# Kernel optimization log

Hardware: AMD Instinct MI355X
Metric: run time of the kernel (lower is better)

## Reference

```python
import jax, jax.numpy as jnp
import numpy as np

N_NODES = 10000
N_EDGES = 160000
IN_CH = 1030
HID = 256
HEADS = 4
OUT_CH = 49
NEG_SLOPE = 0.2
EPS = 1e-5


def setup_inputs() -> dict:
    key = jax.random.key(0)
    ks = jax.random.split(key, 20)
    HC = HID * HEADS  # 1024
    inp = {
        "x": jax.random.normal(ks[0], (N_NODES, IN_CH), dtype=jnp.float32),
        "edge_index": jax.random.randint(ks[1], (2, N_EDGES), 0, N_NODES, dtype=jnp.int64),
        # conv1 (GATv2): lin_l (source), lin_r (target), att, out bias
        "c1_wl": jax.random.normal(ks[2], (IN_CH, HC), dtype=jnp.float32) * 0.03,
        "c1_bl": jnp.zeros((HC,), dtype=jnp.float32),
        "c1_wr": jax.random.normal(ks[3], (IN_CH, HC), dtype=jnp.float32) * 0.03,
        "c1_br": jnp.zeros((HC,), dtype=jnp.float32),
        "c1_att": jax.random.normal(ks[4], (HEADS, HID), dtype=jnp.float32) * 0.06,
        "c1_bias": jnp.zeros((HC,), dtype=jnp.float32),
        # norm1 (per-node LayerNorm over channels)
        "ln1_w": jnp.ones((HC,), dtype=jnp.float32),
        "ln1_b": jnp.zeros((HC,), dtype=jnp.float32),
        # conv2
        "c2_wl": jax.random.normal(ks[5], (HC, HC), dtype=jnp.float32) * 0.03,
        "c2_bl": jnp.zeros((HC,), dtype=jnp.float32),
        "c2_wr": jax.random.normal(ks[6], (HC, HC), dtype=jnp.float32) * 0.03,
        "c2_br": jnp.zeros((HC,), dtype=jnp.float32),
        "c2_att": jax.random.normal(ks[7], (HEADS, HID), dtype=jnp.float32) * 0.06,
        "c2_bias": jnp.zeros((HC,), dtype=jnp.float32),
        # norm2
        "ln2_w": jnp.ones((HC,), dtype=jnp.float32),
        "ln2_b": jnp.zeros((HC,), dtype=jnp.float32),
        # classifier: Linear(HC, HID) -> ELU -> Linear(HID, OUT_CH)
        "cls_w1": jax.random.normal(ks[8], (HC, HID), dtype=jnp.float32) * 0.03,
        "cls_b1": jnp.zeros((HID,), dtype=jnp.float32),
        "cls_w2": jax.random.normal(ks[9], (HID, OUT_CH), dtype=jnp.float32) * 0.06,
        "cls_b2": jnp.zeros((OUT_CH,), dtype=jnp.float32),
    }
    return inp


def gatv2_conv(x, src, dst, wl, bl, wr, br, att, bias, n_nodes):
    """PyG GATv2Conv, concat heads. src/dst include self loops."""
    H, C = att.shape
    xl = (x @ wl + bl).reshape(-1, H, C)  # source transform [N,H,C]
    xr = (x @ wr + br).reshape(-1, H, C)  # target transform [N,H,C]
    m = xl[src] + xr[dst]                  # [E,H,C] gather + add
    e = jnp.einsum("ehc,hc->eh", jax.nn.leaky_relu(m, NEG_SLOPE), att)  # [E,H]
    # segment softmax over destination node
    emax = jax.ops.segment_max(e, dst, num_segments=n_nodes)
    p = jnp.exp(e - emax[dst])
    denom = jax.ops.segment_sum(p, dst, num_segments=n_nodes)
    alpha = p / (denom[dst] + 1e-16)       # [E,H]
    out = jax.ops.segment_sum(xl[src] * alpha[:, :, None], dst, num_segments=n_nodes)
    return out.reshape(n_nodes, H * C) + bias


def layer_norm(x, w, b):
    mu = jnp.mean(x, axis=-1, keepdims=True)
    var = jnp.var(x, axis=-1, keepdims=True)
    return (x - mu) / jnp.sqrt(var + EPS) * w + b


def reference(x, edge_index, c1_wl, c1_bl, c1_wr, c1_br, c1_att, c1_bias,
              ln1_w, ln1_b, c2_wl, c2_bl, c2_wr, c2_br, c2_att, c2_bias,
              ln2_w, ln2_b, cls_w1, cls_b1, cls_w2, cls_b2):
    n = x.shape[0]
    loops = jnp.arange(n, dtype=edge_index.dtype)
    src = jnp.concatenate([edge_index[0], loops])  # add_self_loops=True
    dst = jnp.concatenate([edge_index[1], loops])

    h = gatv2_conv(x, src, dst, c1_wl, c1_bl, c1_wr, c1_br, c1_att, c1_bias, n)
    h = jax.nn.elu(layer_norm(h, ln1_w, ln1_b))
    # dropout: identity at inference
    h = gatv2_conv(h, src, dst, c2_wl, c2_bl, c2_wr, c2_br, c2_att, c2_bias, n)
    h = jax.nn.elu(layer_norm(h, ln2_w, ln2_b))
    h = jax.nn.elu(h @ cls_w1 + cls_b1)
    return h @ cls_w2 + cls_b2  # [N, 49]
```

## Files before the change

### kernel.cpp

```cpp
#include <hip/hip_runtime.h>
#include <stdint.h>

#define N_NODES 10000
#define N_EDGES 160000
#define E_TOT   170000
#define IN_CH   1030
#define HC      1024
#define OUT_CH  49
#define NEG_SLOPE 0.2f
#define LN_EPS 1e-5f
#define LOG2E 1.4426950408889634f

#define MPAD  10112
#define K1PAD 1088

typedef __attribute__((ext_vector_type(8))) __bf16 bf16x8;
typedef __attribute__((ext_vector_type(4))) float floatx4;
typedef __attribute__((ext_vector_type(2))) float floatx2;
typedef _Float16 h2 __attribute__((ext_vector_type(2)));

static __device__ __forceinline__ unsigned short f2bf(float f) {
  union { float f; uint32_t u; } v; v.f = f;
  uint32_t u = v.u;
  u += 0x7fffu + ((u >> 16) & 1u);
  return (unsigned short)(u >> 16);
}
static __device__ __forceinline__ unsigned short f2h(float f) {
  _Float16 h = (_Float16)f;
  union { _Float16 h; unsigned short u; } v; v.h = h; return v.u;
}
static __device__ __forceinline__ h2 bits2h2(uint32_t u) {
  union { uint32_t i; h2 h; } v; v.i = u; return v.h;
}
static __device__ __forceinline__ floatx2 h2f2(h2 a) {
  floatx2 r; r.x = (float)a.x; r.y = (float)a.y; return r;
}

static __device__ __forceinline__ float wred_add(float x) {
#define DPP_ADD(ctrl, rmask)                                                   \
  x += __builtin_bit_cast(float, __builtin_amdgcn_update_dpp(                  \
           0, __builtin_bit_cast(int, x), ctrl, rmask, 0xf, true))
  DPP_ADD(0x111, 0xf);
  DPP_ADD(0x112, 0xf);
  DPP_ADD(0x114, 0xf);
  DPP_ADD(0x118, 0xf);
  DPP_ADD(0x142, 0xa);
  DPP_ADD(0x143, 0xc);
#undef DPP_ADD
  return __builtin_bit_cast(float,
      __builtin_amdgcn_readlane(__builtin_bit_cast(int, x), 63));
}


__global__ void cast_x_kernel(const float* __restrict__ x, unsigned short* __restrict__ xa,
                              int* __restrict__ counts) {
  int idx = blockIdx.x * 256 + threadIdx.x;
  if (idx < N_NODES) counts[idx] = 0;
  if (idx >= N_NODES * K1PAD) return;
  int m = idx / K1PAD, k = idx - m * K1PAD;
  float v = (k < IN_CH) ? x[m * IN_CH + k] : 0.f;
  xa[idx] = f2bf(v);
}

static __device__ __forceinline__ void transpose_body(
    float (*tile)[33], const float* __restrict__ wa, const float* __restrict__ wb,
    int split, int lda, int ldb, int Kvalid, int Kout,
    unsigned short* __restrict__ out, int bx, int by, int t) {
  int n0 = bx * 32, k0 = by * 32;
  int tx = t & 31, ty = t >> 5;
#pragma unroll
  for (int i = 0; i < 4; i++) {
    int k = k0 + ty + i * 8;
    int n = n0 + tx;
    float v = 0.f;
    if (k < Kvalid) v = (n < split) ? wa[(size_t)k * lda + n] : wb[(size_t)k * ldb + (n - split)];
    tile[ty + i * 8][tx] = v;
  }
  __syncthreads();
#pragma unroll
  for (int i = 0; i < 4; i++) {
    int n = n0 + ty + i * 8;
    int k = k0 + tx;
    out[(size_t)n * Kout + k] = f2bf(tile[tx][ty + i * 8]);
  }
}

#define NB_W1 2176
#define NB_W2 2048
#define NB_WC 256
#define NB_CNT 665
__global__ __launch_bounds__(256) void prep2_kernel(
    const float* __restrict__ c1_wl, const float* __restrict__ c1_wr,
    const float* __restrict__ c2_wl, const float* __restrict__ c2_wr,
    const float* __restrict__ cls_w1,
    const int* __restrict__ dstArr, int* __restrict__ counts,
    unsigned short* __restrict__ wt1, unsigned short* __restrict__ wt2,
    unsigned short* __restrict__ wtc1)
{
  __shared__ float tile[32][33];
  int b = blockIdx.x, t = threadIdx.x;
  if (b < NB_W1) {
    transpose_body(tile, c1_wl, c1_wr, 1024, 1024, 1024, IN_CH, K1PAD, wt1, b & 63, b >> 6, t);
  } else if (b < NB_W1 + NB_W2) {
    int bb = b - NB_W1;
    transpose_body(tile, c2_wl, c2_wr, 1024, 1024, 1024, 1024, 1024, wt2, bb & 63, bb >> 6, t);
  } else if (b < NB_W1 + NB_W2 + NB_WC) {
    int bb = b - (NB_W1 + NB_W2);
    transpose_body(tile, cls_w1, cls_w1, 256, 256, 256, 1024, 1024, wtc1, bb & 7, bb >> 3, t);
  } else {
    int e = (b - (NB_W1 + NB_W2 + NB_WC)) * 256 + t;
    if (e < E_TOT) {
      int d = (e < N_EDGES) ? dstArr[e] : (e - N_EDGES);
      atomicAdd(&counts[d], 1);
    }
  }
}

__global__ __launch_bounds__(256) void scan_kernel(const int* __restrict__ counts,
                                                   int* __restrict__ rstart,
                                                   int* __restrict__ rwork) {
  __shared__ int sm[256];
  int t = threadIdx.x;
  int b0 = t * 40;
  int b1 = b0 + 40; if (b1 > N_NODES) b1 = N_NODES; if (b0 > N_NODES) b0 = N_NODES;
  int s = 0;
  for (int i = b0; i < b1; i++) s += counts[i];
  sm[t] = s; __syncthreads();
  for (int st = 1; st < 256; st <<= 1) {
    int add = (t >= st) ? sm[t - st] : 0;
    __syncthreads();
    sm[t] += add;
    __syncthreads();
  }
  int run = sm[t] - s;
  for (int i = b0; i < b1; i++) { rstart[i] = run; rwork[i] = run; run += counts[i]; }
  if (t == 255) rstart[N_NODES] = run;
}

__global__ void scatter_kernel(const int* __restrict__ srcArr, const int* __restrict__ dstArr,
                               int* __restrict__ rwork, int* __restrict__ csrsrc) {
  int e = blockIdx.x * 256 + threadIdx.x;
  if (e >= E_TOT) return;
  if (e < 16) csrsrc[E_TOT + e] = 0;
  int d, sv;
  if (e < N_EDGES) { d = dstArr[e]; sv = srcArr[e]; }
  else { d = e - N_EDGES; sv = d; }
  int pos = atomicAdd(&rwork[d], 1);
  csrsrc[pos] = sv;
}

template <int MODE, int KC>
__global__ __launch_bounds__(256, 4) void gemm_bf16(
    const unsigned short* __restrict__ A, const unsigned short* __restrict__ Bt,
    float* __restrict__ Cf, unsigned short* __restrict__ Cb,
    const float* __restrict__ blo, const float* __restrict__ bhi,
    int M, int ldc, int bsplit)
{
  __shared__ __align__(16) unsigned short As[128 * 64];
  __shared__ __align__(16) unsigned short Bs[128 * 64];
  const int t = threadIdx.x;
  const int w = t >> 6, lane = t & 63;

  const unsigned int nwg = gridDim.x * gridDim.y;
  const unsigned int bid = blockIdx.y * gridDim.x + blockIdx.x;
  const unsigned int q8 = nwg >> 3, r8 = nwg & 7;
  const unsigned int xcd = bid & 7, sub = bid >> 3;
  const unsigned int wg = (xcd < r8 ? xcd * (q8 + 1) : r8 * (q8 + 1) + (xcd - r8) * q8) + sub;
  const int tile_n = (wg % gridDim.x) * 128, tile_m = (wg / gridDim.x) * 128;

  floatx4 acc[4][4] = {};

  const int qq = w * 64 + lane;
  const int row0 = qq >> 3;
  const int gj = (qq & 7) ^ (row0 & 7);
  const unsigned short* gA0 = A  + (size_t)(tile_m + row0) * KC + gj * 8;
  const unsigned short* gB0 = Bt + (size_t)(tile_n + row0) * KC + gj * 8;

  const int wm = (w >> 1) * 64, wn = (w & 1) * 64;
  const int lrow = lane & 15, cg0 = (lane >> 4);
  const int sw = lrow & 7;

#pragma unroll 1
  for (int k0 = 0; k0 < KC; k0 += 64) {
#pragma unroll
    for (int p = 0; p < 4; p++) {
      __builtin_amdgcn_global_load_lds(
          (const __attribute__((address_space(1))) void*)(gA0 + p * 32 * KC),
          (__attribute__((address_space(3))) void*)(As + p * 2048 + w * 512), 16, 0, 0);
      __builtin_amdgcn_global_load_lds(
          (const __attribute__((address_space(1))) void*)(gB0 + p * 32 * KC),
          (__attribute__((address_space(3))) void*)(Bs + p * 2048 + w * 512), 16, 0, 0);
    }
    gA0 += 64; gB0 += 64;
    __syncthreads();
#pragma unroll
    for (int h = 0; h < 2; h++) {
      const int sc = (h * 4 + cg0) ^ sw;
      bf16x8 a[4], b[4];
#pragma unroll
      for (int mi = 0; mi < 4; mi++)
        a[mi] = *(const bf16x8*)(As + (wm + mi * 16 + lrow) * 64 + sc * 8);
#pragma unroll
      for (int ni = 0; ni < 4; ni++)
        b[ni] = *(const bf16x8*)(Bs + (wn + ni * 16 + lrow) * 64 + sc * 8);
#pragma unroll
      for (int mi = 0; mi < 4; mi++)
#pragma unroll
        for (int ni = 0; ni < 4; ni++)
          acc[mi][ni] = __builtin_amdgcn_mfma_f32_16x16x32_bf16(a[mi], b[ni], acc[mi][ni], 0, 0, 0);
    }
    __syncthreads();
  }

  float bcol[4];
#pragma unroll
  for (int ni = 0; ni < 4; ni++) {
    int n = tile_n + wn + ni * 16 + lrow;
    bcol[ni] = (n < bsplit) ? blo[n] : bhi[n - bsplit];
  }

  const int rbase = (lane >> 4) * 4;
#pragma unroll
  for (int mi = 0; mi < 4; mi++) {
#pragma unroll
    for (int r = 0; r < 4; r++) {
      int m = tile_m + wm + mi * 16 + rbase + r;
      if (m >= M) continue;
#pragma unroll
      for (int ni = 0; ni < 4; ni++) {
        int n = tile_n + wn + ni * 16 + lrow;
        float v = acc[mi][ni][r] + bcol[ni];
        if (MODE == 0) {
          Cf[(size_t)m * ldc + n] = v;
        } else if (MODE == 1) {
          Cf[(size_t)m * ldc + n] = v > 0.f ? v : expm1f(v);
        } else {
          Cb[(size_t)m * 2048 + n] = f2h(v);
        }
      }
    }
  }
}


__global__ __launch_bounds__(256) void gat_ln_kernel(
    const unsigned short* __restrict__ xlr,
    const float* __restrict__ att,
    const int* __restrict__ csrsrc, const int* __restrict__ rstart,
    const float* __restrict__ bias,
    const float* __restrict__ lnw, const float* __restrict__ lnb,
    unsigned short* __restrict__ out)
{
  const int d = blockIdx.x;
  const int t = threadIdx.x;
  const int lane = t & 63, wv = t >> 6;
  const int c = wv * 256 + lane * 4;

  uint2 xru = *(const uint2*)(xlr + (size_t)d * 2048 + 1024 + c);
  h2 xr0 = bits2h2(xru.x), xr1 = bits2h2(xru.y);
  float4 aw4 = *(const float4*)(att + c);
  h2 aw0, aw1;
  aw0.x = (_Float16)(aw4.x * LOG2E); aw0.y = (_Float16)(aw4.y * LOG2E);
  aw1.x = (_Float16)(aw4.z * LOG2E); aw1.y = (_Float16)(aw4.w * LOG2E);
  const h2 ns = {(_Float16)NEG_SLOPE, (_Float16)NEG_SLOPE};
  const unsigned short* xbase = xlr + c;

  int start = rstart[d], deg = rstart[d + 1] - start;

  float m = -3.0e38f, l = 0.f;
  floatx2 accA = {0.f, 0.f}, accB = {0.f, 0.f};

  int i = 0;
  if (deg >= 4) {
    int sA0 = csrsrc[start],     sA1 = csrsrc[start + 1];
    int sA2 = csrsrc[start + 2], sA3 = csrsrc[start + 3];
    uint2 uA0 = *(const uint2*)(xbase + (size_t)sA0 * 2048);
    uint2 uA1 = *(const uint2*)(xbase + (size_t)sA1 * 2048);
    uint2 uA2 = *(const uint2*)(xbase + (size_t)sA2 * 2048);
    uint2 uA3 = *(const uint2*)(xbase + (size_t)sA3 * 2048);
    int sB0 = csrsrc[start + 4], sB1 = csrsrc[start + 5];
    int sB2 = csrsrc[start + 6], sB3 = csrsrc[start + 7];
    for (; i + 4 <= deg; i += 4) {
      int sC0 = csrsrc[start + i + 8],  sC1 = csrsrc[start + i + 9];
      int sC2 = csrsrc[start + i + 10], sC3 = csrsrc[start + i + 11];
      uint2 uB0 = *(const uint2*)(xbase + (size_t)sB0 * 2048);
      uint2 uB1 = *(const uint2*)(xbase + (size_t)sB1 * 2048);
      uint2 uB2 = *(const uint2*)(xbase + (size_t)sB2 * 2048);
      uint2 uB3 = *(const uint2*)(xbase + (size_t)sB3 * 2048);

      h2 xh0a = bits2h2(uA0.x), xh0b = bits2h2(uA0.y);
      h2 xh1a = bits2h2(uA1.x), xh1b = bits2h2(uA1.y);
      h2 xh2a = bits2h2(uA2.x), xh2b = bits2h2(uA2.y);
      h2 xh3a = bits2h2(uA3.x), xh3b = bits2h2(uA3.y);
      h2 t0a = xh0a + xr0, t0b = xh0b + xr1;
      h2 t1a = xh1a + xr0, t1b = xh1b + xr1;
      h2 t2a = xh2a + xr0, t2b = xh2b + xr1;
      h2 t3a = xh3a + xr0, t3b = xh3b + xr1;
      h2 r0a = __builtin_elementwise_max(t0a, t0a * ns);
      h2 r0b = __builtin_elementwise_max(t0b, t0b * ns);
      h2 r1a = __builtin_elementwise_max(t1a, t1a * ns);
      h2 r1b = __builtin_elementwise_max(t1b, t1b * ns);
      h2 r2a = __builtin_elementwise_max(t2a, t2a * ns);
      h2 r2b = __builtin_elementwise_max(t2b, t2b * ns);
      h2 r3a = __builtin_elementwise_max(t3a, t3a * ns);
      h2 r3b = __builtin_elementwise_max(t3b, t3b * ns);
      float p0 = __builtin_amdgcn_fdot2(r0b, aw1, __builtin_amdgcn_fdot2(r0a, aw0, 0.f, false), false);
      float p1 = __builtin_amdgcn_fdot2(r1b, aw1, __builtin_amdgcn_fdot2(r1a, aw0, 0.f, false), false);
      float p2 = __builtin_amdgcn_fdot2(r2b, aw1, __builtin_amdgcn_fdot2(r2a, aw0, 0.f, false), false);
      float p3 = __builtin_amdgcn_fdot2(r3b, aw1, __builtin_amdgcn_fdot2(r3a, aw0, 0.f, false), false);
      p0 = wred_add(p0);
      p1 = wred_add(p1);
      p2 = wred_add(p2);
      p3 = wred_add(p3);
      float mx = fmaxf(fmaxf(p0, p1), fmaxf(p2, p3));
      if (mx > m) {
        float sc = exp2f(m - mx);
        floatx2 scv; scv.x = sc; scv.y = sc;
        accA *= scv; accB *= scv; l *= sc;
        m = mx;
      }
      float pe0 = exp2f(p0 - m), pe1 = exp2f(p1 - m);
      float pe2 = exp2f(p2 - m), pe3 = exp2f(p3 - m);
      floatx2 x0A = h2f2(xh0a), x0B = h2f2(xh0b);
      floatx2 x1A = h2f2(xh1a), x1B = h2f2(xh1b);
      floatx2 x2A = h2f2(xh2a), x2B = h2f2(xh2b);
      floatx2 x3A = h2f2(xh3a), x3B = h2f2(xh3b);
      floatx2 v0; v0.x = pe0; v0.y = pe0;
      floatx2 v1; v1.x = pe1; v1.y = pe1;
      floatx2 v2; v2.x = pe2; v2.y = pe2;
      floatx2 v3; v3.x = pe3; v3.y = pe3;
      accA += x0A * v0; accA += x1A * v1; accA += x2A * v2; accA += x3A * v3;
      accB += x0B * v0; accB += x1B * v1; accB += x2B * v2; accB += x3B * v3;
      l += pe0 + pe1 + pe2 + pe3;

      uA0 = uB0; uA1 = uB1; uA2 = uB2; uA3 = uB3;
      sB0 = sC0; sB1 = sC1; sB2 = sC2; sB3 = sC3;
    }
  }
  for (; i < deg; i++) {
    int s0 = csrsrc[start + i];
    uint2 u0 = *(const uint2*)(xbase + (size_t)s0 * 2048);
    h2 xh0a = bits2h2(u0.x), xh0b = bits2h2(u0.y);
    h2 t0a = xh0a + xr0, t0b = xh0b + xr1;
    h2 r0a = __builtin_elementwise_max(t0a, t0a * ns);
    h2 r0b = __builtin_elementwise_max(t0b, t0b * ns);
    float p0 = __builtin_amdgcn_fdot2(r0b, aw1, __builtin_amdgcn_fdot2(r0a, aw0, 0.f, false), false);
    p0 = wred_add(p0);
    if (p0 > m) {
      float sc = exp2f(m - p0);
      floatx2 scv; scv.x = sc; scv.y = sc;
      accA *= scv; accB *= scv; l *= sc;
      m = p0;
    }
    float pe0 = exp2f(p0 - m);
    floatx2 x0A = h2f2(xh0a), x0B = h2f2(xh0b);
    floatx2 pe0v; pe0v.x = pe0; pe0v.y = pe0;
    accA += x0A * pe0v;
    accB += x0B * pe0v;
    l += pe0;
  }

  float rd = 1.f / (l + 1e-16f);
  float4 bv = *(const float4*)(bias + c);
  float o0 = accA.x * rd + bv.x, o1 = accA.y * rd + bv.y;
  float o2 = accB.x * rd + bv.z, o3 = accB.y * rd + bv.w;

  __shared__ float ws1[4], ws2[4];
  float s1 = o0 + o1 + o2 + o3;
  float s2 = o0 * o0 + o1 * o1 + o2 * o2 + o3 * o3;
#pragma unroll
  for (int mm = 32; mm >= 1; mm >>= 1) {
    s1 += __shfl_xor(s1, mm, 64);
    s2 += __shfl_xor(s2, mm, 64);
  }
  if (lane == 0) { ws1[wv] = s1; ws2[wv] = s2; }
  __syncthreads();
  float mean = (ws1[0] + ws1[1] + ws1[2] + ws1[3]) * (1.f / 1024.f);
  float var  = (ws2[0] + ws2[1] + ws2[2] + ws2[3]) * (1.f / 1024.f) - mean * mean;
  float rstd = rsqrtf(var + LN_EPS);
  float4 wv4 = *(const float4*)(lnw + c);
  float4 bb  = *(const float4*)(lnb + c);
  float z0 = (o0 - mean) * rstd * wv4.x + bb.x; z0 = z0 > 0.f ? z0 : expm1f(z0);
  float z1 = (o1 - mean) * rstd * wv4.y + bb.y; z1 = z1 > 0.f ? z1 : expm1f(z1);
  float z2 = (o2 - mean) * rstd * wv4.z + bb.z; z2 = z2 > 0.f ? z2 : expm1f(z2);
  float z3 = (o3 - mean) * rstd * wv4.w + bb.w; z3 = z3 > 0.f ? z3 : expm1f(z3);
  ushort4 u;
  u.x = f2bf(z0); u.y = f2bf(z1); u.z = f2bf(z2); u.w = f2bf(z3);
  *(ushort4*)(out + (size_t)d * 1024 + c) = u;
}


__global__ __launch_bounds__(256) void cls2_kernel(
    const float* __restrict__ h3, const float* __restrict__ w2,
    const float* __restrict__ b2, float* __restrict__ out)
{
  __shared__ float row[4][256];
  int t = threadIdx.x, wv = t >> 6, lane = t & 63;
  int node = blockIdx.x * 4 + wv;
  *(float4*)(&row[wv][lane * 4]) = *(const float4*)(h3 + (size_t)node * 256 + lane * 4);
  __syncthreads();
  if (lane < OUT_CH) {
    float a0 = 0.f, a1 = 0.f, a2 = 0.f, a3 = 0.f;
#pragma unroll 4
    for (int k = 0; k < 256; k += 4) {
      a0 += row[wv][k]     * w2[(k    ) * OUT_CH + lane];
      a1 += row[wv][k + 1] * w2[(k + 1) * OUT_CH + lane];
      a2 += row[wv][k + 2] * w2[(k + 2) * OUT_CH + lane];
      a3 += row[wv][k + 3] * w2[(k + 3) * OUT_CH + lane];
    }
    out[node * OUT_CH + lane] = (a0 + a1) + (a2 + a3) + b2[lane];
  }
}


extern "C" void kernel_launch(void* const* d_in, const int* in_sizes, int n_in,
                              void* d_out, int out_size, void* d_ws, size_t ws_size,
                              hipStream_t stream)
{
  const float* x       = (const float*)d_in[0];
  const int*   ei      = (const int*)d_in[1];
  const float* c1_wl   = (const float*)d_in[2];
  const float* c1_bl   = (const float*)d_in[3];
  const float* c1_wr   = (const float*)d_in[4];
  const float* c1_br   = (const float*)d_in[5];
  const float* c1_att  = (const float*)d_in[6];
  const float* c1_bias = (const float*)d_in[7];
  const float* ln1_w   = (const float*)d_in[8];
  const float* ln1_b   = (const float*)d_in[9];
  const float* c2_wl   = (const float*)d_in[10];
  const float* c2_bl   = (const float*)d_in[11];
  const float* c2_wr   = (const float*)d_in[12];
  const float* c2_br   = (const float*)d_in[13];
  const float* c2_att  = (const float*)d_in[14];
  const float* c2_bias = (const float*)d_in[15];
  const float* ln2_w   = (const float*)d_in[16];
  const float* ln2_b   = (const float*)d_in[17];
  const float* cls_w1  = (const float*)d_in[18];
  const float* cls_b1  = (const float*)d_in[19];
  const float* cls_w2  = (const float*)d_in[20];
  const float* cls_b2  = (const float*)d_in[21];

  const int* srcArr = ei;
  const int* dstArr = ei + N_EDGES;

  char* ws = (char*)d_ws;
  size_t off = 0;
  auto alloc = [&](size_t bytes) { void* p = ws + off; off += (bytes + 255) & ~(size_t)255; return p; };
  unsigned short* xa      = (unsigned short*)alloc((size_t)MPAD * K1PAD * 2);
  unsigned short* wt1     = (unsigned short*)alloc((size_t)2048 * K1PAD * 2);
  unsigned short* wt2     = (unsigned short*)alloc((size_t)2048 * 1024 * 2);
  unsigned short* wtc1    = (unsigned short*)alloc((size_t)256 * 1024 * 2);
  unsigned short* xlr     = (unsigned short*)alloc((size_t)N_NODES * 2048 * 2);
  float*          h3      = (float*)alloc((size_t)N_NODES * 256 * 4);
  unsigned short* hb      = (unsigned short*)alloc((size_t)MPAD * 1024 * 2);
  int*            counts  = (int*)alloc(N_NODES * 4);
  int*            rwork   = (int*)alloc(N_NODES * 4);
  int*            rstart  = (int*)alloc((N_NODES + 1) * 4);
  int*            csrsrc  = (int*)alloc((E_TOT + 16) * 4);
  (void)in_sizes; (void)n_in; (void)out_size; (void)ws_size;

  cast_x_kernel<<<(N_NODES * K1PAD + 255) / 256, 256, 0, stream>>>(x, xa, counts);
  prep2_kernel<<<NB_W1 + NB_W2 + NB_WC + NB_CNT, 256, 0, stream>>>(
      c1_wl, c1_wr, c2_wl, c2_wr, cls_w1, dstArr, counts, wt1, wt2, wtc1);

  scan_kernel<<<1, 256, 0, stream>>>(counts, rstart, rwork);
  scatter_kernel<<<(E_TOT + 255) / 256, 256, 0, stream>>>(srcArr, dstArr, rwork, csrsrc);

  gemm_bf16<2, K1PAD><<<dim3(16, 79), 256, 0, stream>>>(xa, wt1, nullptr, xlr, c1_bl, c1_br, N_NODES, 0, 1024);
  gat_ln_kernel<<<N_NODES, 256, 0, stream>>>(xlr, c1_att, csrsrc, rstart, c1_bias, ln1_w, ln1_b, hb);

  gemm_bf16<2, 1024><<<dim3(16, 79), 256, 0, stream>>>(hb, wt2, nullptr, xlr, c2_bl, c2_br, N_NODES, 0, 1024);
  gat_ln_kernel<<<N_NODES, 256, 0, stream>>>(xlr, c2_att, csrsrc, rstart, c2_bias, ln2_w, ln2_b, hb);

  gemm_bf16<1, 1024><<<dim3(2, 79), 256, 0, stream>>>(hb, wtc1, h3, nullptr, cls_b1, cls_b1, N_NODES, 256, 1024);
  cls2_kernel<<<2500, 256, 0, stream>>>(h3, cls_w2, cls_b2, (float*)d_out);
}
```

Before: 458.6 us.

## Add 128x256-tile 512-thread GEMM with LDS double buffering for GAT projections

Adds a new bf16 MFMA GEMM kernel that uses 128x256 output tiles, 8 waves, direct global-to-LDS loads, a double-buffered K pipeline with explicit waitcnt and barrier scheduling, and XCD-aware tile mapping. It replaces the 128x128 GEMM for both GAT layer projections. The larger N tile raises operand reuse and halves A-tile reloads, and the pipelining overlaps loads with MFMA work. The output buffer is padded to MPAD rows because the new kernel writes without bounds checks. The 96KB of dynamic LDS and 512 threads per block may limit occupancy.

```diff
diff --git a/kernel.cpp b/kernel.cpp
--- a/kernel.cpp
+++ b/kernel.cpp
@@ -147,6 +147,137 @@
   else { d = e - N_EDGES; sv = d; }
   int pos = atomicAdd(&rwork[d], 1);
   csrsrc[pos] = sv;
+}
+
+
+extern __shared__ unsigned short smem256[];
+
+template <int KC>
+__global__ __launch_bounds__(512, 2) void gemm256(
+    const unsigned short* __restrict__ A,
+    const unsigned short* __restrict__ Bt,
+    unsigned short* __restrict__ Cb,
+    const float* __restrict__ blo, const float* __restrict__ bhi)
+{
+  constexpr int NT = KC / 64;
+  unsigned short* As = smem256;
+  unsigned short* Bs = smem256 + 2 * 8192;
+
+  const int tid = threadIdx.x;
+  const int w = tid >> 6, lane = tid & 63;
+  const int wm = w >> 2, wn = w & 3;
+
+  const unsigned int bid = blockIdx.y * gridDim.x + blockIdx.x;
+  const unsigned int wg = (bid & 7) * 79u + (bid >> 3);
+  const int tile_n = (int)(wg % 8u) * 256;
+  const int tile_m = (int)(wg / 8u) * 128;
+
+  const int rq = tid >> 3;
+  const int gc = (tid & 7) ^ (rq & 7);
+  const unsigned short* gA = A  + (size_t)(tile_m + rq) * KC + gc * 8;
+  const unsigned short* gB = Bt + (size_t)(tile_n + rq) * KC + gc * 8;
+  const int ldsw = w * 512;
+
+  const int lrow = lane & 15, cg0 = lane >> 4, sw = lrow & 7;
+
+  floatx4 acc[4][4] = {};
+
+#define STAGE_A(kt, p2)                                                          \
+  __builtin_amdgcn_global_load_lds(                                              \
+      (const __attribute__((address_space(1))) void*)(gA + (size_t)(p2) * 64 * KC + (kt) * 64), \
+      (__attribute__((address_space(3))) void*)(As + ((kt) & 1) * 8192 + (p2) * 4096 + ldsw), 16, 0, 0)
+#define STAGE_B(kt, s)                                                           \
+  __builtin_amdgcn_global_load_lds(                                              \
+      (const __attribute__((address_space(1))) void*)(gB + (size_t)(s) * 64 * KC + (kt) * 64),  \
+      (__attribute__((address_space(3))) void*)(Bs + ((kt) & 1) * 16384 + (s) * 4096 + ldsw), 16, 0, 0)
+
+  STAGE_B(0, 0); STAGE_B(0, 1); STAGE_A(0, 0);
+  STAGE_B(0, 2); STAGE_B(0, 3); STAGE_A(0, 1);
+
+  bf16x8 b[4][2], a[2][2];
+
+#pragma unroll 1
+  for (int t = 0; t < NT; ++t) {
+    const unsigned short* Ac = As + (t & 1) * 8192;
+    const unsigned short* Bc = Bs + (t & 1) * 16384;
+    const bool st = (t + 1 < NT);
+
+    asm volatile("s_waitcnt vmcnt(1)" ::: "memory");
+    __builtin_amdgcn_s_barrier();
+    asm volatile("" ::: "memory");
+    __builtin_amdgcn_sched_barrier(0);
+
+#pragma unroll
+    for (int n = 0; n < 4; ++n)
+#pragma unroll
+      for (int kh = 0; kh < 2; ++kh)
+        b[n][kh] = *(const bf16x8*)(Bc + (wn * 64 + n * 16 + lrow) * 64 + (((kh << 2) | cg0) ^ sw) * 8);
+#pragma unroll
+    for (int f = 0; f < 2; ++f)
+#pragma unroll
+      for (int kh = 0; kh < 2; ++kh)
+        a[f][kh] = *(const bf16x8*)(Ac + (f * 32 + wm * 16 + lrow) * 64 + (((kh << 2) | cg0) ^ sw) * 8);
+    if (st) { STAGE_B(t + 1, 0); STAGE_B(t + 1, 1); STAGE_A(t + 1, 0); }
+    __builtin_amdgcn_s_barrier();
+    asm volatile("s_waitcnt lgkmcnt(0)" ::: "memory");
+    __builtin_amdgcn_sched_barrier(0);
+    __builtin_amdgcn_s_setprio(1);
+#pragma unroll
+    for (int f = 0; f < 2; ++f)
+#pragma unroll
+      for (int n = 0; n < 4; ++n) {
+        acc[f][n] = __builtin_amdgcn_mfma_f32_16x16x32_bf16(a[f][0], b[n][0], acc[f][n], 0, 0, 0);
+        acc[f][n] = __builtin_amdgcn_mfma_f32_16x16x32_bf16(a[f][1], b[n][1], acc[f][n], 0, 0, 0);
+      }
+    __builtin_amdgcn_s_setprio(0);
+
+    if (st) asm volatile("s_waitcnt vmcnt(3)" ::: "memory");
+    else    asm volatile("s_waitcnt vmcnt(0)" ::: "memory");
+    __builtin_amdgcn_s_barrier();
+    asm volatile("" ::: "memory");
+    __builtin_amdgcn_sched_barrier(0);
+
+#pragma unroll
+    for (int f = 0; f < 2; ++f)
+#pragma unroll
+      for (int kh = 0; kh < 2; ++kh)
+        a[f][kh] = *(const bf16x8*)(Ac + ((f + 2) * 32 + wm * 16 + lrow) * 64 + (((kh << 2) | cg0) ^ sw) * 8);
+    if (st) { STAGE_B(t + 1, 2); STAGE_B(t + 1, 3); STAGE_A(t + 1, 1); }
+    __builtin_amdgcn_s_barrier();
+    asm volatile("s_waitcnt lgkmcnt(0)" ::: "memory");
+    __builtin_amdgcn_sched_barrier(0);
+    __builtin_amdgcn_s_setprio(1);
+#pragma unroll
+    for (int f = 0; f < 2; ++f)
+#pragma unroll
+      for (int n = 0; n < 4; ++n) {
+        acc[f + 2][n] = __builtin_amdgcn_mfma_f32_16x16x32_bf16(a[f][0], b[n][0], acc[f + 2][n], 0, 0, 0);
+        acc[f + 2][n] = __builtin_amdgcn_mfma_f32_16x16x32_bf16(a[f][1], b[n][1], acc[f + 2][n], 0, 0, 0);
+      }
+    __builtin_amdgcn_s_setprio(0);
+  }
+#undef STAGE_A
+#undef STAGE_B
+
+  const int rbase = cg0 * 4;
+  float bcol[4];
+#pragma unroll
+  for (int n = 0; n < 4; ++n) {
+    int col = tile_n + wn * 64 + n * 16 + lrow;
+    bcol[n] = (col < 1024) ? blo[col] : bhi[col - 1024];
+  }
+#pragma unroll
+  for (int f = 0; f < 4; ++f) {
+    const int mrow = tile_m + f * 32 + wm * 16 + rbase;
+#pragma unroll
+    for (int r = 0; r < 4; ++r) {
+#pragma unroll
+      for (int n = 0; n < 4; ++n) {
+        int col = tile_n + wn * 64 + n * 16 + lrow;
+        Cb[(size_t)(mrow + r) * 2048 + col] = f2h(acc[f][n][r] + bcol[n]);
+      }
+    }
+  }
 }
 
 template <int MODE, int KC>
@@ -450,7 +581,7 @@
   unsigned short* wt1     = (unsigned short*)alloc((size_t)2048 * K1PAD * 2);
   unsigned short* wt2     = (unsigned short*)alloc((size_t)2048 * 1024 * 2);
   unsigned short* wtc1    = (unsigned short*)alloc((size_t)256 * 1024 * 2);
-  unsigned short* xlr     = (unsigned short*)alloc((size_t)N_NODES * 2048 * 2);
+  unsigned short* xlr     = (unsigned short*)alloc((size_t)MPAD * 2048 * 2);
   float*          h3      = (float*)alloc((size_t)N_NODES * 256 * 4);
   unsigned short* hb      = (unsigned short*)alloc((size_t)MPAD * 1024 * 2);
   int*            counts  = (int*)alloc(N_NODES * 4);
@@ -466,10 +597,10 @@
   scan_kernel<<<1, 256, 0, stream>>>(counts, rstart, rwork);
   scatter_kernel<<<(E_TOT + 255) / 256, 256, 0, stream>>>(srcArr, dstArr, rwork, csrsrc);
 
-  gemm_bf16<2, K1PAD><<<dim3(16, 79), 256, 0, stream>>>(xa, wt1, nullptr, xlr, c1_bl, c1_br, N_NODES, 0, 1024);
+  gemm256<K1PAD><<<dim3(8, 79), 512, 98304, stream>>>(xa, wt1, xlr, c1_bl, c1_br);
   gat_ln_kernel<<<N_NODES, 256, 0, stream>>>(xlr, c1_att, csrsrc, rstart, c1_bias, ln1_w, ln1_b, hb);
 
-  gemm_bf16<2, 1024><<<dim3(16, 79), 256, 0, stream>>>(hb, wt2, nullptr, xlr, c2_bl, c2_br, N_NODES, 0, 1024);
+  gemm256<1024><<<dim3(8, 79), 512, 98304, stream>>>(hb, wt2, xlr, c2_bl, c2_br);
   gat_ln_kernel<<<N_NODES, 256, 0, stream>>>(xlr, c2_att, csrsrc, rstart, c2_bias, ln2_w, ln2_b, hb);
 
   gemm_bf16<1, 1024><<<dim3(2, 79), 256, 0, stream>>>(hb, wtc1, h3, nullptr, cls_b1, cls_b1, N_NODES, 256, 1024);
```

Result: slower. 490.9 us (+7.0%).

## Fuse classifier MLP into one MFMA kernel and vectorize input cast

Applied to the files above, without the earlier changes.

Replaces the classifier's bf16 GEMM plus scalar second-layer kernel with one kernel. It computes the first linear layer with MFMA, applies bias and ELU, stages the fp16 result in LDS, and does the second 256x49 layer with f16 MFMA against a pre-transposed padded weight. This removes the fp32 intermediate round trip through global memory and one launch, at the cost of fewer, larger blocks (79 blocks of 128 rows). The x-to-bf16 cast kernel is also vectorized to process four elements per thread.

```diff
diff --git a/kernel.cpp b/kernel.cpp
--- a/kernel.cpp
+++ b/kernel.cpp
@@ -15,6 +15,7 @@
 #define K1PAD 1088
 
 typedef __attribute__((ext_vector_type(8))) __bf16 bf16x8;
+typedef __attribute__((ext_vector_type(8))) _Float16 h8;
 typedef __attribute__((ext_vector_type(4))) float floatx4;
 typedef __attribute__((ext_vector_type(2))) float floatx2;
 typedef _Float16 h2 __attribute__((ext_vector_type(2)));
@@ -56,16 +57,27 @@
                               int* __restrict__ counts) {
   int idx = blockIdx.x * 256 + threadIdx.x;
   if (idx < N_NODES) counts[idx] = 0;
-  if (idx >= N_NODES * K1PAD) return;
-  int m = idx / K1PAD, k = idx - m * K1PAD;
-  float v = (k < IN_CH) ? x[m * IN_CH + k] : 0.f;
-  xa[idx] = f2bf(v);
+  if (idx >= N_NODES * (K1PAD / 4)) return;
+  int m = idx / (K1PAD / 4), k4 = idx - m * (K1PAD / 4);
+  int k = k4 * 4;
+  ushort4 o;
+  if (k + 3 < IN_CH) {
+    float2 v0 = *(const float2*)(x + (size_t)m * IN_CH + k);
+    float2 v1 = *(const float2*)(x + (size_t)m * IN_CH + k + 2);
+    o.x = f2bf(v0.x); o.y = f2bf(v0.y); o.z = f2bf(v1.x); o.w = f2bf(v1.y);
+  } else {
+    o.x = (k     < IN_CH) ? f2bf(x[(size_t)m * IN_CH + k    ]) : (unsigned short)0;
+    o.y = (k + 1 < IN_CH) ? f2bf(x[(size_t)m * IN_CH + k + 1]) : (unsigned short)0;
+    o.z = (k + 2 < IN_CH) ? f2bf(x[(size_t)m * IN_CH + k + 2]) : (unsigned short)0;
+    o.w = (unsigned short)0;
+  }
+  *(ushort4*)(xa + (size_t)m * K1PAD + k) = o;
 }
 
 static __device__ __forceinline__ void transpose_body(
     float (*tile)[33], const float* __restrict__ wa, const float* __restrict__ wb,
     int split, int lda, int ldb, int Kvalid, int Kout,
-    unsigned short* __restrict__ out, int bx, int by, int t) {
+    unsigned short* __restrict__ out, int bx, int by, int t, bool f16o) {
   int n0 = bx * 32, k0 = by * 32;
   int tx = t & 31, ty = t >> 5;
 #pragma unroll
@@ -73,7 +85,10 @@
     int k = k0 + ty + i * 8;
     int n = n0 + tx;
     float v = 0.f;
-    if (k < Kvalid) v = (n < split) ? wa[(size_t)k * lda + n] : wb[(size_t)k * ldb + (n - split)];
+    if (k < Kvalid) {
+      if (n < split) v = wa[(size_t)k * lda + n];
+      else if (ldb)  v = wb[(size_t)k * ldb + (n - split)];
+    }
     tile[ty + i * 8][tx] = v;
   }
   __syncthreads();
@@ -81,34 +96,39 @@
   for (int i = 0; i < 4; i++) {
     int n = n0 + ty + i * 8;
     int k = k0 + tx;
-    out[(size_t)n * Kout + k] = f2bf(tile[tx][ty + i * 8]);
+    float v = tile[tx][ty + i * 8];
+    out[(size_t)n * Kout + k] = f16o ? f2h(v) : f2bf(v);
   }
 }
 
 #define NB_W1 2176
 #define NB_W2 2048
 #define NB_WC 256
+#define NB_WC2 16
 #define NB_CNT 665
 __global__ __launch_bounds__(256) void prep2_kernel(
     const float* __restrict__ c1_wl, const float* __restrict__ c1_wr,
     const float* __restrict__ c2_wl, const float* __restrict__ c2_wr,
-    const float* __restrict__ cls_w1,
+    const float* __restrict__ cls_w1, const float* __restrict__ cls_w2,
     const int* __restrict__ dstArr, int* __restrict__ counts,
     unsigned short* __restrict__ wt1, unsigned short* __restrict__ wt2,
-    unsigned short* __restrict__ wtc1)
+    unsigned short* __restrict__ wtc1, unsigned short* __restrict__ wtc2)
 {
   __shared__ float tile[32][33];
   int b = blockIdx.x, t = threadIdx.x;
   if (b < NB_W1) {
-    transpose_body(tile, c1_wl, c1_wr, 1024, 1024, 1024, IN_CH, K1PAD, wt1, b & 63, b >> 6, t);
+    transpose_body(tile, c1_wl, c1_wr, 1024, 1024, 1024, IN_CH, K1PAD, wt1, b & 63, b >> 6, t, false);
   } else if (b < NB_W1 + NB_W2) {
     int bb = b - NB_W1;
-    transpose_body(tile, c2_wl, c2_wr, 1024, 1024, 1024, 1024, 1024, wt2, bb & 63, bb >> 6, t);
+    transpose_body(tile, c2_wl, c2_wr, 1024, 1024, 1024, 1024, 1024, wt2, bb & 63, bb >> 6, t, false);
   } else if (b < NB_W1 + NB_W2 + NB_WC) {
     int bb = b - (NB_W1 + NB_W2);
-    transpose_body(tile, cls_w1, cls_w1, 256, 256, 256, 1024, 1024, wtc1, bb & 7, bb >> 3, t);
+    transpose_body(tile, cls_w1, cls_w1, 256, 256, 256, 1024, 1024, wtc1, bb & 7, bb >> 3, t, false);
+  } else if (b < NB_W1 + NB_W2 + NB_WC + NB_WC2) {
+    int bb = b - (NB_W1 + NB_W2 + NB_WC);
+    transpose_body(tile, cls_w2, cls_w2, OUT_CH, OUT_CH, 0, 256, 256, wtc2, bb & 1, bb >> 1, t, true);
   } else {
-    int e = (b - (NB_W1 + NB_W2 + NB_WC)) * 256 + t;
+    int e = (b - (NB_W1 + NB_W2 + NB_WC + NB_WC2)) * 256 + t;
     if (e < E_TOT) {
       int d = (e < N_EDGES) ? dstArr[e] : (e - N_EDGES);
       atomicAdd(&counts[d], 1);
@@ -390,25 +410,127 @@
 }
 
 
-__global__ __launch_bounds__(256) void cls2_kernel(
-    const float* __restrict__ h3, const float* __restrict__ w2,
-    const float* __restrict__ b2, float* __restrict__ out)
+extern __shared__ unsigned short clssm[];
+
+__global__ __launch_bounds__(256) void cls_fused_kernel(
+    const unsigned short* __restrict__ A,
+    const unsigned short* __restrict__ Bt,
+    const float* __restrict__ b1,
+    const unsigned short* __restrict__ w2t,
+    const float* __restrict__ b2,
+    float* __restrict__ out)
 {
-  __shared__ float row[4][256];
-  int t = threadIdx.x, wv = t >> 6, lane = t & 63;
-  int node = blockIdx.x * 4 + wv;
-  *(float4*)(&row[wv][lane * 4]) = *(const float4*)(h3 + (size_t)node * 256 + lane * 4);
+  unsigned short* As = clssm;
+  unsigned short* Bs = clssm + 8192;
+  unsigned short* hbuf = clssm;
+
+  const int t = threadIdx.x;
+  const int w = t >> 6, lane = t & 63;
+  const int tile_m = blockIdx.x * 128;
+
+  const int q = w * 64 + lane;
+  const int row0 = q >> 3;
+  const int gj = (q & 7) ^ (row0 & 7);
+  const unsigned short* gA0 = A  + (size_t)(tile_m + row0) * 1024 + gj * 8;
+  const unsigned short* gB0 = Bt + (size_t)row0 * 1024 + gj * 8;
+
+  const int wm = (w >> 1) * 64, wn = (w & 1) * 128;
+  const int lrow = lane & 15, cg0 = lane >> 4, sw = lrow & 7;
+
+  floatx4 acc[4][8] = {};
+
+#pragma unroll 1
+  for (int k0 = 0; k0 < 1024; k0 += 64) {
+#pragma unroll
+    for (int p = 0; p < 4; p++)
+      __builtin_amdgcn_global_load_lds(
+          (const __attribute__((address_space(1))) void*)(gA0 + p * 32 * 1024),
+          (__attribute__((address_space(3))) void*)(As + p * 2048 + w * 512), 16, 0, 0);
+#pragma unroll
+    for (int s = 0; s < 8; s++)
+      __builtin_amdgcn_global_load_lds(
+          (const __attribute__((address_space(1))) void*)(gB0 + s * 32 * 1024),
+          (__attribute__((address_space(3))) void*)(Bs + s * 2048 + w * 512), 16, 0, 0);
+    gA0 += 64; gB0 += 64;
+    __syncthreads();
+#pragma unroll
+    for (int h = 0; h < 2; h++) {
+      const int sc = ((h << 2) | cg0) ^ sw;
+      bf16x8 a[4], b[8];
+#pragma unroll
+      for (int mi = 0; mi < 4; mi++) {
+        int ar = wm + mi * 16 + lrow;
+        a[mi] = *(const bf16x8*)(As + (ar >> 5) * 2048 + (ar & 31) * 64 + sc * 8);
+      }
+#pragma unroll
+      for (int ni = 0; ni < 8; ni++) {
+        int br = wn + ni * 16 + lrow;
+        b[ni] = *(const bf16x8*)(Bs + (br >> 5) * 2048 + (br & 31) * 64 + sc * 8);
+      }
+#pragma unroll
+      for (int mi = 0; mi < 4; mi++)
+#pragma unroll
+        for (int ni = 0; ni < 8; ni++)
+          acc[mi][ni] = __builtin_amdgcn_mfma_f32_16x16x32_bf16(a[mi], b[ni], acc[mi][ni], 0, 0, 0);
+    }
+    __syncthreads();
+  }
+
+  float bcol[8];
+#pragma unroll
+  for (int ni = 0; ni < 8; ni++) bcol[ni] = b1[wn + ni * 16 + lrow];
+  const int rbase = cg0 * 4;
+#pragma unroll
+  for (int mi = 0; mi < 4; mi++) {
+#pragma unroll
+    for (int r = 0; r < 4; r++) {
+      int row = wm + mi * 16 + rbase + r;
+#pragma unroll
+      for (int ni = 0; ni < 8; ni++) {
+        int col = wn + ni * 16 + lrow;
+        float v = acc[mi][ni][r] + bcol[ni];
+        v = v > 0.f ? v : expm1f(v);
+        int kc = (col >> 3) ^ (row & 7);
+        hbuf[row * 256 + kc * 8 + (col & 7)] = f2h(v);
+      }
+    }
+  }
   __syncthreads();
-  if (lane < OUT_CH) {
-    float a0 = 0.f, a1 = 0.f, a2 = 0.f, a3 = 0.f;
-#pragma unroll 4
-    for (int k = 0; k < 256; k += 4) {
-      a0 += row[wv][k]     * w2[(k    ) * OUT_CH + lane];
-      a1 += row[wv][k + 1] * w2[(k + 1) * OUT_CH + lane];
-      a2 += row[wv][k + 2] * w2[(k + 2) * OUT_CH + lane];
-      a3 += row[wv][k + 3] * w2[(k + 3) * OUT_CH + lane];
-    }
-    out[node * OUT_CH + lane] = (a0 + a1) + (a2 + a3) + b2[lane];
+
+  floatx4 acc3[2][4] = {};
+#pragma unroll
+  for (int kst = 0; kst < 8; kst++) {
+    h8 a3[2], b3[4];
+#pragma unroll
+    for (int mi = 0; mi < 2; mi++) {
+      int ar = w * 32 + mi * 16 + lrow;
+      int kc = (kst * 4 + cg0) ^ (ar & 7);
+      a3[mi] = *(const h8*)(hbuf + ar * 256 + kc * 8);
+    }
+#pragma unroll
+    for (int ni = 0; ni < 4; ni++) {
+      int br = ni * 16 + lrow;
+      b3[ni] = *(const h8*)(w2t + br * 256 + kst * 32 + cg0 * 8);
+    }
+#pragma unroll
+    for (int mi = 0; mi < 2; mi++)
+#pragma unroll
+      for (int ni = 0; ni < 4; ni++)
+        acc3[mi][ni] = __builtin_amdgcn_mfma_f32_16x16x32_f16(a3[mi], b3[ni], acc3[mi][ni], 0, 0, 0);
+  }
+#pragma unroll
+  for (int mi = 0; mi < 2; mi++) {
+    int rb = tile_m + w * 32 + mi * 16 + rbase;
+#pragma unroll
+    for (int r = 0; r < 4; r++) {
+      int node = rb + r;
+      if (node >= N_NODES) continue;
+#pragma unroll
+      for (int ni = 0; ni < 4; ni++) {
+        int j = ni * 16 + lrow;
+        if (j < OUT_CH) out[(size_t)node * OUT_CH + j] = acc3[mi][ni][r] + b2[j];
+      }
+    }
   }
 }
 
@@ -450,8 +572,8 @@
   unsigned short* wt1     = (unsigned short*)alloc((size_t)2048 * K1PAD * 2);
   unsigned short* wt2     = (unsigned short*)alloc((size_t)2048 * 1024 * 2);
   unsigned short* wtc1    = (unsigned short*)alloc((size_t)256 * 1024 * 2);
+  unsigned short* wtc2    = (unsigned short*)alloc((size_t)64 * 256 * 2);
   unsigned short* xlr     = (unsigned short*)alloc((size_t)N_NODES * 2048 * 2);
-  float*          h3      = (float*)alloc((size_t)N_NODES * 256 * 4);
   unsigned short* hb      = (unsigned short*)alloc((size_t)MPAD * 1024 * 2);
   int*            counts  = (int*)alloc(N_NODES * 4);
   int*            rwork   = (int*)alloc(N_NODES * 4);
@@ -459,9 +581,9 @@
   int*            csrsrc  = (int*)alloc((E_TOT + 16) * 4);
   (void)in_sizes; (void)n_in; (void)out_size; (void)ws_size;
 
-  cast_x_kernel<<<(N_NODES * K1PAD + 255) / 256, 256, 0, stream>>>(x, xa, counts);
-  prep2_kernel<<<NB_W1 + NB_W2 + NB_WC + NB_CNT, 256, 0, stream>>>(
-      c1_wl, c1_wr, c2_wl, c2_wr, cls_w1, dstArr, counts, wt1, wt2, wtc1);
+  cast_x_kernel<<<(N_NODES * (K1PAD / 4) + 255) / 256, 256, 0, stream>>>(x, xa, counts);
+  prep2_kernel<<<NB_W1 + NB_W2 + NB_WC + NB_WC2 + NB_CNT, 256, 0, stream>>>(
+      c1_wl, c1_wr, c2_wl, c2_wr, cls_w1, cls_w2, dstArr, counts, wt1, wt2, wtc1, wtc2);
 
   scan_kernel<<<1, 256, 0, stream>>>(counts, rstart, rwork);
   scatter_kernel<<<(E_TOT + 255) / 256, 256, 0, stream>>>(srcArr, dstArr, rwork, csrsrc);
@@ -472,6 +594,5 @@
   gemm_bf16<2, 1024><<<dim3(16, 79), 256, 0, stream>>>(hb, wt2, nullptr, xlr, c2_bl, c2_br, N_NODES, 0, 1024);
   gat_ln_kernel<<<N_NODES, 256, 0, stream>>>(xlr, c2_att, csrsrc, rstart, c2_bias, ln2_w, ln2_b, hb);
 
-  gemm_bf16<1, 1024><<<dim3(2, 79), 256, 0, stream>>>(hb, wtc1, h3, nullptr, cls_b1, cls_b1, N_NODES, 256, 1024);
-  cls2_kernel<<<2500, 256, 0, stream>>>(h3, cls_w2, cls_b2, (float*)d_out);
-}
+  cls_fused_kernel<<<79, 256, 65536, stream>>>(hb, wtc1, cls_b1, wtc2, cls_b2, (float*)d_out);
+}
```

Measured after the change: 450.8 us. Within noise of the previous version (-1.7%).
